# Performance work log

Hardware: AMD Instinct MI355X
Metric: run time of the kernel (lower is better)

## Reference

```python
import jax, jax.numpy as jnp
import numpy as np

B, N, D = 32, 4096, 128
H = D // 2      # GRU hidden = 64
Q = D // 4      # MLP hidden = 32
HORIZON = 28


def setup_inputs() -> dict:
    key = jax.random.key(0)
    ks = jax.random.split(key, 16)
    s = lambda k, shape, fan: jax.random.normal(k, shape, jnp.float32) * (1.0 / np.sqrt(fan))
    return {
        "features": jax.random.normal(ks[0], (B, N, D), jnp.float32),
        "last_value": jax.random.uniform(ks[1], (B, N), jnp.float32),
        # GRU (input_size=1, hidden=H), PyTorch gate order r,z,n
        "W_ih": s(ks[2], (3 * H, 1), 1),
        "W_hh": s(ks[3], (3 * H, H), H),
        "b_ih": s(ks[4], (3 * H,), H),
        "b_hh": s(ks[5], (3 * H,), H),
        # hidden_proj: Linear(D -> H)
        "Wp": s(ks[6], (H, D), D), "bp": s(ks[7], (H,), D),
        # output_proj: Linear(H->Q), ReLU, Linear(Q->1)
        "Wo1": s(ks[8], (Q, H), H), "bo1": s(ks[9], (Q,), H),
        "Wo2": s(ks[10], (1, Q), Q), "bo2": s(ks[11], (1,), Q),
        # refine_gate: Linear(D->Q), ReLU, Linear(Q->horizon), Sigmoid
        "Wg1": s(ks[12], (Q, D), D), "bg1": s(ks[13], (Q,), D),
        "Wg2": s(ks[14], (HORIZON, Q), Q), "bg2": s(ks[15], (HORIZON,), Q),
        "log_decay": jnp.asarray(-2.3, jnp.float32),
    }


def reference(features, last_value, W_ih, W_hh, b_ih, b_hh, Wp, bp,
              Wo1, bo1, Wo2, bo2, Wg1, bg1, Wg2, bg2, log_decay):
    b, n, d = features.shape
    h0 = features.reshape(b * n, d) @ Wp.T + bp          # [BN, H]
    x0 = last_value.reshape(b * n, 1)                    # [BN, 1]

    def step(carry, _):
        h, x = carry
        gi = x @ W_ih.T + b_ih                           # [BN, 3H]
        gh = h @ W_hh.T + b_hh                           # [BN, 3H]
        r = jax.nn.sigmoid(gi[:, :H] + gh[:, :H])
        z = jax.nn.sigmoid(gi[:, H:2 * H] + gh[:, H:2 * H])
        ncell = jnp.tanh(gi[:, 2 * H:] + r * gh[:, 2 * H:])
        h_new = (1.0 - z) * ncell + z * h
        pred = jax.nn.relu(h_new @ Wo1.T + bo1) @ Wo2.T + bo2  # [BN, 1] (dropout = eval)
        return (h_new, pred), pred[:, 0]

    (_, _), preds = jax.lax.scan(step, (h0, x0), None, length=HORIZON)
    gru_pred = preds.T.reshape(b, n, HORIZON)            # [B, N, horizon]

    gate = jax.nn.sigmoid(jax.nn.relu(features @ Wg1.T + bg1) @ Wg2.T + bg2)
    t = jnp.arange(1, HORIZON + 1, dtype=jnp.float32)
    decay_curve = jnp.exp(-jnp.exp(log_decay) * t)       # [horizon]
    decay_pred = last_value[..., None] * decay_curve
    return gate * gru_pred + (1.0 - gate) * decay_pred
```

## Files before the change

kernel.cpp:

```cpp
#include <hip/hip_runtime.h>

#define TPB 256
#define HOR 28
#define LOG2E 1.44269504088896340736f

typedef _Float16 f16;
typedef __attribute__((ext_vector_type(2))) _Float16 f16x2;
typedef __attribute__((ext_vector_type(4))) _Float16 f16x4;
typedef __attribute__((ext_vector_type(8))) _Float16 f16x8;
typedef __attribute__((ext_vector_type(4))) float f32x4;

union V8 { f16x8 v8; f16x4 v4[2]; f16x2 h2[4]; };

#define MFMA16(A,B,C) __builtin_amdgcn_mfma_f32_16x16x32_f16((A),(B),(C),0,0,0)

__device__ __forceinline__ f16x2 pk2(float a, float b) {
    return __builtin_bit_cast(f16x2, __builtin_amdgcn_cvt_pkrtz(a, b));
}

#define WS 68

__global__ __launch_bounds__(TPB, 4) void predictor_kernel(
    const float* __restrict__ features,
    const float* __restrict__ last_value,
    const float* __restrict__ W_ih,
    const float* __restrict__ W_hh,
    const float* __restrict__ b_ih,
    const float* __restrict__ b_hh,
    const float* __restrict__ Wp,
    const float* __restrict__ bp,
    const float* __restrict__ Wo1,
    const float* __restrict__ bo1,
    const float* __restrict__ Wo2,
    const float* __restrict__ bo2,
    const float* __restrict__ Wg1,
    const float* __restrict__ bg1,
    const float* __restrict__ Wg2,
    const float* __restrict__ bg2,
    const float* __restrict__ log_decay,
    float* __restrict__ out)
{
    __shared__ __align__(16) f16 s_mem[16000];

    const int tid = threadIdx.x;
    const int wv = tid >> 6, ln = tid & 63;
    const int a = ln & 15, g = ln >> 4;
    const int row0 = blockIdx.x * 64 + wv * 16;

    const f32x4 ZF = {0.f, 0.f, 0.f, 0.f};
    const f16x2 Z2 = {(f16)0.f, (f16)0.f};
    const f16x4 ZH4 = {(f16)0.f, (f16)0.f, (f16)0.f, (f16)0.f};

    f16* s_wp  = s_mem;
    f16* s_wg1 = s_mem + 8704;
    f16* s_wg2 = s_mem + 13056;

    for (int i = tid; i < 64 * 128; i += TPB) s_wp [(i >> 7) * 136 + (i & 127)] = (f16)Wp[i];
    for (int i = tid; i < 32 * 128; i += TPB) s_wg1[(i >> 7) * 136 + (i & 127)] = (f16)Wg1[i];
    for (int i = tid; i < 32 * 32; i += TPB) {
        int t = i >> 5, s = i & 31;
        int q = ((s >> 2) & 1) * 16 + ((s >> 3) & 3) * 4 + (s & 3);
        s_wg2[t * 40 + s] = (f16)((t < HOR) ? Wg2[t * 32 + q] : 0.0f);
    }

    f16x2 bH[4][2];
    #pragma unroll
    for (int c = 0; c < 4; ++c)
        #pragma unroll
        for (int p = 0; p < 2; ++p) {
            int u0 = c * 16 + g * 4 + 2 * p;
            bH[c][p] = pk2(b_hh[128 + u0] * 2.0f * LOG2E, b_hh[128 + u0 + 1] * 2.0f * LOG2E);
        }
    f16x2 bo1q[2][2], wo2q[2][2];
    #pragma unroll
    for (int mt = 0; mt < 2; ++mt)
        #pragma unroll
        for (int p = 0; p < 2; ++p) {
            int q0 = mt * 16 + g * 4 + 2 * p;
            bo1q[mt][p] = pk2(bo1[q0], bo1[q0 + 1]);
            wo2q[mt][p] = pk2(Wo2[q0], Wo2[q0 + 1]);
        }
    const float bo2v = bo2[0];
    const float edc  = LOG2E * __builtin_amdgcn_exp2f(LOG2E * log_decay[0]);
    const float lv   = last_value[row0 + a];
    const bool  g0   = (g == 0);

    V8 FF[4];
    #pragma unroll
    for (int kt = 0; kt < 4; ++kt) {
        const float* fp = features + (size_t)(row0 + a) * 128 + kt * 32 + g * 8;
        f32x4 v0 = *(const f32x4*)fp;
        f32x4 v1 = *(const f32x4*)(fp + 4);
        FF[kt].h2[0] = pk2(v0[0], v0[1]); FF[kt].h2[1] = pk2(v0[2], v0[3]);
        FF[kt].h2[2] = pk2(v1[0], v1[1]); FF[kt].h2[3] = pk2(v1[2], v1[3]);
    }

    __syncthreads();

    f32x4 h4[4];
    {
        f16x2 bpq[4][2];
        #pragma unroll
        for (int c = 0; c < 4; ++c)
            #pragma unroll
            for (int p = 0; p < 2; ++p) {
                int u0 = c * 16 + g * 4 + 2 * p;
                bpq[c][p] = pk2(bp[u0], bp[u0 + 1]);
            }
        #pragma unroll
        for (int nt = 0; nt < 4; ++nt) {
            f32x4 acc = ZF;
            #pragma unroll
            for (int kt = 0; kt < 4; ++kt) {
                f16x8 w = *(const f16x8*)&s_wp[(nt * 16 + a) * 136 + kt * 32 + g * 8];
                acc = MFMA16(w, FF[kt].v8, acc);
            }
            #pragma unroll
            for (int r = 0; r < 4; ++r) acc[r] += (float)bpq[nt][r >> 1][r & 1];
            h4[nt] = acc;
        }
    }

    float gA0, gA1, gA2, gA3, gB0, gB1, gB2, gB3;
    {
        f32x4 a1acc[2];
        #pragma unroll
        for (int mt = 0; mt < 2; ++mt) {
            f32x4 acc = ZF;
            #pragma unroll
            for (int kt = 0; kt < 4; ++kt) {
                f16x8 w = *(const f16x8*)&s_wg1[(mt * 16 + a) * 136 + kt * 32 + g * 8];
                acc = MFMA16(w, FF[kt].v8, acc);
            }
            #pragma unroll
            for (int r = 0; r < 4; ++r) {
                int q0 = mt * 16 + g * 4 + r;
                acc[r] = fmaxf(acc[r] + bg1[q0], 0.f);
            }
            a1acc[mt] = acc;
        }
        V8 A1;
        A1.h2[0] = pk2(a1acc[0][0], a1acc[0][1]);
        A1.h2[1] = pk2(a1acc[0][2], a1acc[0][3]);
        A1.h2[2] = pk2(a1acc[1][0], a1acc[1][1]);
        A1.h2[3] = pk2(a1acc[1][2], a1acc[1][3]);
        float gv[2][4];
        #pragma unroll
        for (int mt = 0; mt < 2; ++mt) {
            f32x4 acc = ZF;
            f16x8 w = *(const f16x8*)&s_wg2[(mt * 16 + a) * 40 + g * 8];
            acc = MFMA16(w, A1.v8, acc);
            #pragma unroll
            for (int r = 0; r < 4; ++r) {
                int t0 = mt * 16 + g * 4 + r;
                float lg = acc[r] + ((t0 < HOR) ? bg2[t0] : 0.f);
                gv[mt][r] = __builtin_amdgcn_rcpf(1.0f + __builtin_amdgcn_exp2f(-LOG2E * lg));
            }
        }
        gA0 = gv[0][0]; gA1 = gv[0][1]; gA2 = gv[0][2]; gA3 = gv[0][3];
        gB0 = gv[1][0]; gB1 = gv[1][1]; gB2 = gv[1][2]; gB3 = gv[1][3];
    }

    __syncthreads();
    f16* s_whh = s_mem;
    f16* s_wo1 = s_mem + 13056;
    f16* s_wx  = s_mem + 15232;
    for (int i = tid; i < 192 * WS; i += TPB) {
        int rr = i / WS, cc = i - rr * WS;
        float s = (rr < 128) ? -LOG2E : 2.0f * LOG2E;
        s_whh[i] = (f16)((cc < 64) ? W_hh[rr * 64 + cc] * s : 0.0f);
    }
    for (int i = tid; i < 32 * WS; i += TPB) {
        int rr = i / WS, cc = i - rr * WS;
        s_wo1[i] = (f16)((cc < 64) ? Wo1[rr * 64 + cc] : 0.0f);
    }
    for (int i = tid; i < 192; i += TPB) {
        float s = (i < 128) ? -LOG2E : 2.0f * LOG2E;
        s_wx[i * 4 + 0] = (f16)(W_ih[i] * s);
        s_wx[i * 4 + 1] = (f16)(((i < 128) ? (b_ih[i] + b_hh[i]) : b_ih[i]) * s);
        s_wx[i * 4 + 2] = (f16)0.f;
        s_wx[i * 4 + 3] = (f16)0.f;
    }
    __syncthreads();

    const int wr = a * WS + 4 * g;

    V8 F0, F1, F2;
    F0.h2[0] = pk2(h4[0][0], h4[0][1]); F0.h2[1] = pk2(h4[0][2], h4[0][3]);
    F0.h2[2] = pk2(h4[1][0], h4[1][1]); F0.h2[3] = pk2(h4[1][2], h4[1][3]);
    F1.h2[0] = pk2(h4[2][0], h4[2][1]); F1.h2[1] = pk2(h4[2][2], h4[2][3]);
    F1.h2[2] = pk2(h4[3][0], h4[3][1]); F1.h2[3] = pk2(h4[3][2], h4[3][3]);
    F2.h2[0] = Z2; F2.h2[1] = Z2; F2.h2[2] = Z2; F2.h2[3] = Z2;

    float x = lv;

#define GATE3(ACC, BR, c) do { \
        V8 w0_, w1_, w2_; \
        const int rw_ = BR + (c) * 16 + a; \
        const int rb_ = (BR + (c) * 16) * WS + wr; \
        w0_.v4[0] = *(const f16x4*)&s_whh[rb_]; \
        w0_.v4[1] = *(const f16x4*)&s_whh[rb_ + 16]; \
        w1_.v4[0] = *(const f16x4*)&s_whh[rb_ + 32]; \
        w1_.v4[1] = *(const f16x4*)&s_whh[rb_ + 48]; \
        w2_.v4[0] = *(const f16x4*)&s_wx[rw_ * 4]; \
        w2_.v4[1] = ZH4; \
        ACC = MFMA16(w0_.v8, F0.v8, ZF); \
        ACC = MFMA16(w1_.v8, F1.v8, ACC); \
        ACC = MFMA16(w2_.v8, F2.v8, ACC); } while (0)

#define GATEN(ACC, ACC2, c) do { \
        V8 w0_, w1_, w2_; \
        const int rw_ = 128 + (c) * 16 + a; \
        const int rb_ = (128 + (c) * 16) * WS + wr; \
        w0_.v4[0] = *(const f16x4*)&s_whh[rb_]; \
        w0_.v4[1] = *(const f16x4*)&s_whh[rb_ + 16]; \
        w1_.v4[0] = *(const f16x4*)&s_whh[rb_ + 32]; \
        w1_.v4[1] = *(const f16x4*)&s_whh[rb_ + 48]; \
        w2_.v4[0] = *(const f16x4*)&s_wx[rw_ * 4]; \
        w2_.v4[1] = ZH4; \
        ACC = MFMA16(w0_.v8, F0.v8, ZF); \
        ACC = MFMA16(w1_.v8, F1.v8, ACC); \
        ACC2 = MFMA16(w2_.v8, F2.v8, ZF); } while (0)

#define GRU_CELL(c, AR, AZ, AN, AN2) do { \
        _Pragma("unroll") \
        for (int p = 0; p < 2; ++p) { \
            _Pragma("unroll") \
            for (int q = 0; q < 2; ++q) { \
                int r = p * 2 + q; \
                float rg = __builtin_amdgcn_rcpf(1.0f + __builtin_amdgcn_exp2f(AR[r])); \
                float pb = 1.0f + __builtin_amdgcn_exp2f(AZ[r]); \
                float ghn = AN[r] + (float)bH[c][p][q]; \
                float E  = __builtin_amdgcn_exp2f(fmaf(rg, ghn, AN2[r])); \
                float pE = 1.0f + E; \
                float rD = __builtin_amdgcn_rcpf(pb * pE); \
                float zg = rD * pE; \
                float ivE = rD * pb; \
                float nc = fmaf(-2.0f, ivE, 1.0f); \
                float hv = h4[c][r]; \
                h4[c][r] = fmaf(zg, hv - nc, nc); \
            } \
        } } while (0)

    #pragma unroll 1
    for (int t = 0; t < HOR; ++t) {
        asm volatile("" ::: "memory");
        f16x2 x1 = pk2(x, 1.0f);
        F2.h2[0] = g0 ? x1 : Z2;

        f32x4 aR0, aZ0, aN0, aN20, aR1, aZ1, aN1, aN21;
        GATE3(aR0, 0, 0); GATE3(aZ0, 64, 0); GATEN(aN0, aN20, 0);
        GATE3(aR1, 0, 1); GATE3(aZ1, 64, 1); GATEN(aN1, aN21, 1);
        GRU_CELL(0, aR0, aZ0, aN0, aN20);
        GRU_CELL(1, aR1, aZ1, aN1, aN21);
        GATE3(aR0, 0, 2); GATE3(aZ0, 64, 2); GATEN(aN0, aN20, 2);
        GATE3(aR1, 0, 3); GATE3(aZ1, 64, 3); GATEN(aN1, aN21, 3);
        GRU_CELL(2, aR0, aZ0, aN0, aN20);
        GRU_CELL(3, aR1, aZ1, aN1, aN21);

        F0.h2[0] = pk2(h4[0][0], h4[0][1]); F0.h2[1] = pk2(h4[0][2], h4[0][3]);
        F0.h2[2] = pk2(h4[1][0], h4[1][1]); F0.h2[3] = pk2(h4[1][2], h4[1][3]);
        F1.h2[0] = pk2(h4[2][0], h4[2][1]); F1.h2[1] = pk2(h4[2][2], h4[2][3]);
        F1.h2[2] = pk2(h4[3][0], h4[3][1]); F1.h2[3] = pk2(h4[3][2], h4[3][3]);

        V8 wo;
        f32x4 o0 = ZF, o1 = ZF;
        wo.v4[0] = *(const f16x4*)&s_wo1[wr];
        wo.v4[1] = *(const f16x4*)&s_wo1[wr + 16];
        o0 = MFMA16(wo.v8, F0.v8, o0);
        wo.v4[0] = *(const f16x4*)&s_wo1[wr + 32];
        wo.v4[1] = *(const f16x4*)&s_wo1[wr + 48];
        o0 = MFMA16(wo.v8, F1.v8, o0);
        wo.v4[0] = *(const f16x4*)&s_wo1[16 * WS + wr];
        wo.v4[1] = *(const f16x4*)&s_wo1[16 * WS + wr + 16];
        o1 = MFMA16(wo.v8, F0.v8, o1);
        wo.v4[0] = *(const f16x4*)&s_wo1[16 * WS + wr + 32];
        wo.v4[1] = *(const f16x4*)&s_wo1[16 * WS + wr + 48];
        o1 = MFMA16(wo.v8, F1.v8, o1);

        float part = 0.f;
        #pragma unroll
        for (int p = 0; p < 2; ++p)
            #pragma unroll
            for (int q = 0; q < 2; ++q) {
                int r = 2 * p + q;
                part += fmaxf(o0[r] + (float)bo1q[0][p][q], 0.f) * (float)wo2q[0][p][q];
                part += fmaxf(o1[r] + (float)bo1q[1][p][q], 0.f) * (float)wo2q[1][p][q];
            }
        part += __shfl_xor(part, 16);
        part += __shfl_xor(part, 32);
        float pred = part + bo2v;

        if (g == ((t >> 2) & 3)) {
            float s01 = (t & 1) ? ((t & 16) ? gB1 : gA1) : ((t & 16) ? gB0 : gA0);
            float s23 = (t & 1) ? ((t & 16) ? gB3 : gA3) : ((t & 16) ? gB2 : gA2);
            float gvf = (t & 2) ? s23 : s01;
            float dc = __builtin_amdgcn_exp2f(-edc * (float)(t + 1));
            float lvdc = lv * dc;
            out[(size_t)(row0 + a) * HOR + t] = fmaf(gvf, pred - lvdc, lvdc);
        }
        x = pred;
    }
#undef GATE3
#undef GATEN
#undef GRU_CELL
}

extern "C" void kernel_launch(void* const* d_in, const int* in_sizes, int n_in,
                              void* d_out, int out_size, void* d_ws, size_t ws_size,
                              hipStream_t stream) {
    const float* features   = (const float*)d_in[0];
    const float* last_value = (const float*)d_in[1];
    const float* W_ih       = (const float*)d_in[2];
    const float* W_hh       = (const float*)d_in[3];
    const float* b_ih       = (const float*)d_in[4];
    const float* b_hh       = (const float*)d_in[5];
    const float* Wp         = (const float*)d_in[6];
    const float* bp         = (const float*)d_in[7];
    const float* Wo1        = (const float*)d_in[8];
    const float* bo1        = (const float*)d_in[9];
    const float* Wo2        = (const float*)d_in[10];
    const float* bo2        = (const float*)d_in[11];
    const float* Wg1        = (const float*)d_in[12];
    const float* bg1        = (const float*)d_in[13];
    const float* Wg2        = (const float*)d_in[14];
    const float* bg2        = (const float*)d_in[15];
    const float* log_decay  = (const float*)d_in[16];
    float* out = (float*)d_out;

    dim3 grid(131072 / 64), block(TPB);
    predictor_kernel<<<grid, block, 0, stream>>>(
        features, last_value, W_ih, W_hh, b_ih, b_hh, Wp, bp,
        Wo1, bo1, Wo2, bo2, Wg1, bg1, Wg2, bg2, log_decay, out);
}
```

Measured before the change: 257.1 us.

## Process two 16-row tiles per wave to reuse GRU weight loads

```diff
diff --git a/kernel.cpp b/kernel.cpp
--- a/kernel.cpp
+++ b/kernel.cpp
@@ -17,10 +17,13 @@
 __device__ __forceinline__ f16x2 pk2(float a, float b) {
     return __builtin_bit_cast(f16x2, __builtin_amdgcn_cvt_pkrtz(a, b));
 }
+__device__ __forceinline__ float sigm_pos(float lg) {
+    return __builtin_amdgcn_rcpf(1.0f + __builtin_amdgcn_exp2f(-LOG2E * lg));
+}
 
 #define WS 68
 
-__global__ __launch_bounds__(TPB, 4) void predictor_kernel(
+__global__ __launch_bounds__(TPB, 3) void predictor_kernel(
     const float* __restrict__ features,
     const float* __restrict__ last_value,
     const float* __restrict__ W_ih,
@@ -45,7 +48,7 @@
     const int tid = threadIdx.x;
     const int wv = tid >> 6, ln = tid & 63;
     const int a = ln & 15, g = ln >> 4;
-    const int row0 = blockIdx.x * 64 + wv * 16;
+    const int row0 = blockIdx.x * 128 + wv * 32;
 
     const f32x4 ZF = {0.f, 0.f, 0.f, 0.f};
     const f16x2 Z2 = {(f16)0.f, (f16)0.f};
@@ -82,84 +85,86 @@
         }
     const float bo2v = bo2[0];
     const float edc  = LOG2E * __builtin_amdgcn_exp2f(LOG2E * log_decay[0]);
-    const float lv   = last_value[row0 + a];
+    const float lvA  = last_value[row0 + a];
+    const float lvB  = last_value[row0 + 16 + a];
     const bool  g0   = (g == 0);
 
-    V8 FF[4];
-    #pragma unroll
-    for (int kt = 0; kt < 4; ++kt) {
-        const float* fp = features + (size_t)(row0 + a) * 128 + kt * 32 + g * 8;
-        f32x4 v0 = *(const f32x4*)fp;
-        f32x4 v1 = *(const f32x4*)(fp + 4);
-        FF[kt].h2[0] = pk2(v0[0], v0[1]); FF[kt].h2[1] = pk2(v0[2], v0[3]);
-        FF[kt].h2[2] = pk2(v1[0], v1[1]); FF[kt].h2[3] = pk2(v1[2], v1[3]);
-    }
-
     __syncthreads();
 
-    f32x4 h4[4];
-    {
-        f16x2 bpq[4][2];
-        #pragma unroll
-        for (int c = 0; c < 4; ++c)
-            #pragma unroll
-            for (int p = 0; p < 2; ++p) {
-                int u0 = c * 16 + g * 4 + 2 * p;
-                bpq[c][p] = pk2(bp[u0], bp[u0 + 1]);
-            }
-        #pragma unroll
-        for (int nt = 0; nt < 4; ++nt) {
-            f32x4 acc = ZF;
-            #pragma unroll
-            for (int kt = 0; kt < 4; ++kt) {
-                f16x8 w = *(const f16x8*)&s_wp[(nt * 16 + a) * 136 + kt * 32 + g * 8];
-                acc = MFMA16(w, FF[kt].v8, acc);
-            }
-            #pragma unroll
-            for (int r = 0; r < 4; ++r) acc[r] += (float)bpq[nt][r >> 1][r & 1];
-            h4[nt] = acc;
-        }
-    }
-
-    float gA0, gA1, gA2, gA3, gB0, gB1, gB2, gB3;
-    {
-        f32x4 a1acc[2];
-        #pragma unroll
-        for (int mt = 0; mt < 2; ++mt) {
-            f32x4 acc = ZF;
-            #pragma unroll
-            for (int kt = 0; kt < 4; ++kt) {
-                f16x8 w = *(const f16x8*)&s_wg1[(mt * 16 + a) * 136 + kt * 32 + g * 8];
-                acc = MFMA16(w, FF[kt].v8, acc);
-            }
-            #pragma unroll
-            for (int r = 0; r < 4; ++r) {
-                int q0 = mt * 16 + g * 4 + r;
-                acc[r] = fmaxf(acc[r] + bg1[q0], 0.f);
-            }
-            a1acc[mt] = acc;
-        }
-        V8 A1;
-        A1.h2[0] = pk2(a1acc[0][0], a1acc[0][1]);
-        A1.h2[1] = pk2(a1acc[0][2], a1acc[0][3]);
-        A1.h2[2] = pk2(a1acc[1][0], a1acc[1][1]);
-        A1.h2[3] = pk2(a1acc[1][2], a1acc[1][3]);
-        float gv[2][4];
-        #pragma unroll
-        for (int mt = 0; mt < 2; ++mt) {
-            f32x4 acc = ZF;
-            f16x8 w = *(const f16x8*)&s_wg2[(mt * 16 + a) * 40 + g * 8];
-            acc = MFMA16(w, A1.v8, acc);
-            #pragma unroll
-            for (int r = 0; r < 4; ++r) {
-                int t0 = mt * 16 + g * 4 + r;
-                float lg = acc[r] + ((t0 < HOR) ? bg2[t0] : 0.f);
-                gv[mt][r] = __builtin_amdgcn_rcpf(1.0f + __builtin_amdgcn_exp2f(-LOG2E * lg));
-            }
-        }
-        gA0 = gv[0][0]; gA1 = gv[0][1]; gA2 = gv[0][2]; gA3 = gv[0][3];
-        gB0 = gv[1][0]; gB1 = gv[1][1]; gB2 = gv[1][2]; gB3 = gv[1][3];
-    }
+    f32x4 h4A[4], h4B[4];
+    float ga0, ga1, ga2, ga3, ga4, ga5, ga6, ga7;
+    float gb0, gb1, gb2, gb3, gb4, gb5, gb6, gb7;
+
+#define PHASE1(H4, G0_, G1_, G2_, G3_, G4_, G5_, G6_, G7_, ROFF) do { \
+    V8 FF0, FF1, FF2, FF3; \
+    { \
+        const float* fb_ = features + (size_t)(row0 + (ROFF) + a) * 128 + g * 8; \
+        f32x4 v0, v1; \
+        v0 = *(const f32x4*)(fb_);       v1 = *(const f32x4*)(fb_ + 4); \
+        FF0.h2[0]=pk2(v0[0],v0[1]); FF0.h2[1]=pk2(v0[2],v0[3]); FF0.h2[2]=pk2(v1[0],v1[1]); FF0.h2[3]=pk2(v1[2],v1[3]); \
+        v0 = *(const f32x4*)(fb_ + 32);  v1 = *(const f32x4*)(fb_ + 36); \
+        FF1.h2[0]=pk2(v0[0],v0[1]); FF1.h2[1]=pk2(v0[2],v0[3]); FF1.h2[2]=pk2(v1[0],v1[1]); FF1.h2[3]=pk2(v1[2],v1[3]); \
+        v0 = *(const f32x4*)(fb_ + 64);  v1 = *(const f32x4*)(fb_ + 68); \
+        FF2.h2[0]=pk2(v0[0],v0[1]); FF2.h2[1]=pk2(v0[2],v0[3]); FF2.h2[2]=pk2(v1[0],v1[1]); FF2.h2[3]=pk2(v1[2],v1[3]); \
+        v0 = *(const f32x4*)(fb_ + 96);  v1 = *(const f32x4*)(fb_ + 100); \
+        FF3.h2[0]=pk2(v0[0],v0[1]); FF3.h2[1]=pk2(v0[2],v0[3]); FF3.h2[2]=pk2(v1[0],v1[1]); FF3.h2[3]=pk2(v1[2],v1[3]); \
+    } \
+    _Pragma("unroll") \
+    for (int nt = 0; nt < 4; ++nt) { \
+        f32x4 acc = ZF; \
+        const f16* wp_ = &s_wp[(nt * 16 + a) * 136 + g * 8]; \
+        acc = MFMA16(*(const f16x8*)(wp_),       FF0.v8, acc); \
+        acc = MFMA16(*(const f16x8*)(wp_ + 32),  FF1.v8, acc); \
+        acc = MFMA16(*(const f16x8*)(wp_ + 64),  FF2.v8, acc); \
+        acc = MFMA16(*(const f16x8*)(wp_ + 96),  FF3.v8, acc); \
+        _Pragma("unroll") \
+        for (int r = 0; r < 4; ++r) acc[r] += bp[nt * 16 + g * 4 + r]; \
+        H4[nt] = acc; \
+    } \
+    f32x4 a1_0, a1_1; \
+    { \
+        f32x4 acc = ZF; \
+        const f16* wg_ = &s_wg1[a * 136 + g * 8]; \
+        acc = MFMA16(*(const f16x8*)(wg_),       FF0.v8, acc); \
+        acc = MFMA16(*(const f16x8*)(wg_ + 32),  FF1.v8, acc); \
+        acc = MFMA16(*(const f16x8*)(wg_ + 64),  FF2.v8, acc); \
+        acc = MFMA16(*(const f16x8*)(wg_ + 96),  FF3.v8, acc); \
+        _Pragma("unroll") \
+        for (int r = 0; r < 4; ++r) acc[r] = fmaxf(acc[r] + bg1[g * 4 + r], 0.f); \
+        a1_0 = acc; \
+    } \
+    { \
+        f32x4 acc = ZF; \
+        const f16* wg_ = &s_wg1[(16 + a) * 136 + g * 8]; \
+        acc = MFMA16(*(const f16x8*)(wg_),       FF0.v8, acc); \
+        acc = MFMA16(*(const f16x8*)(wg_ + 32),  FF1.v8, acc); \
+        acc = MFMA16(*(const f16x8*)(wg_ + 64),  FF2.v8, acc); \
+        acc = MFMA16(*(const f16x8*)(wg_ + 96),  FF3.v8, acc); \
+        _Pragma("unroll") \
+        for (int r = 0; r < 4; ++r) acc[r] = fmaxf(acc[r] + bg1[16 + g * 4 + r], 0.f); \
+        a1_1 = acc; \
+    } \
+    V8 A1_; \
+    A1_.h2[0] = pk2(a1_0[0], a1_0[1]); A1_.h2[1] = pk2(a1_0[2], a1_0[3]); \
+    A1_.h2[2] = pk2(a1_1[0], a1_1[1]); A1_.h2[3] = pk2(a1_1[2], a1_1[3]); \
+    { \
+        f32x4 ac0 = ZF, ac1 = ZF; \
+        ac0 = MFMA16(*(const f16x8*)&s_wg2[a * 40 + g * 8],        A1_.v8, ac0); \
+        ac1 = MFMA16(*(const f16x8*)&s_wg2[(16 + a) * 40 + g * 8], A1_.v8, ac1); \
+        G0_ = sigm_pos(ac0[0] + bg2[g * 4 + 0]); \
+        G1_ = sigm_pos(ac0[1] + bg2[g * 4 + 1]); \
+        G2_ = sigm_pos(ac0[2] + bg2[g * 4 + 2]); \
+        G3_ = sigm_pos(ac0[3] + bg2[g * 4 + 3]); \
+        int t4_ = 16 + g * 4; \
+        G4_ = sigm_pos(ac1[0] + ((t4_ + 0 < HOR) ? bg2[t4_ + 0] : 0.f)); \
+        G5_ = sigm_pos(ac1[1] + ((t4_ + 1 < HOR) ? bg2[t4_ + 1] : 0.f)); \
+        G6_ = sigm_pos(ac1[2] + ((t4_ + 2 < HOR) ? bg2[t4_ + 2] : 0.f)); \
+        G7_ = sigm_pos(ac1[3] + ((t4_ + 3 < HOR) ? bg2[t4_ + 3] : 0.f)); \
+    } } while (0)
+
+    PHASE1(h4A, ga0, ga1, ga2, ga3, ga4, ga5, ga6, ga7, 0);
+    PHASE1(h4B, gb0, gb1, gb2, gb3, gb4, gb5, gb6, gb7, 16);
+#undef PHASE1
 
     __syncthreads();
     f16* s_whh = s_mem;
@@ -185,44 +190,52 @@
 
     const int wr = a * WS + 4 * g;
 
-    V8 F0, F1, F2;
-    F0.h2[0] = pk2(h4[0][0], h4[0][1]); F0.h2[1] = pk2(h4[0][2], h4[0][3]);
-    F0.h2[2] = pk2(h4[1][0], h4[1][1]); F0.h2[3] = pk2(h4[1][2], h4[1][3]);
-    F1.h2[0] = pk2(h4[2][0], h4[2][1]); F1.h2[1] = pk2(h4[2][2], h4[2][3]);
-    F1.h2[2] = pk2(h4[3][0], h4[3][1]); F1.h2[3] = pk2(h4[3][2], h4[3][3]);
-    F2.h2[0] = Z2; F2.h2[1] = Z2; F2.h2[2] = Z2; F2.h2[3] = Z2;
-
-    float x = lv;
-
-#define GATE3(ACC, BR, c) do { \
+    V8 F0A, F1A, F0B, F1B, F2A, F2B;
+#define PACKF(F0_, F1_, H4) do { \
+    F0_.h2[0] = pk2(H4[0][0], H4[0][1]); F0_.h2[1] = pk2(H4[0][2], H4[0][3]); \
+    F0_.h2[2] = pk2(H4[1][0], H4[1][1]); F0_.h2[3] = pk2(H4[1][2], H4[1][3]); \
+    F1_.h2[0] = pk2(H4[2][0], H4[2][1]); F1_.h2[1] = pk2(H4[2][2], H4[2][3]); \
+    F1_.h2[2] = pk2(H4[3][0], H4[3][1]); F1_.h2[3] = pk2(H4[3][2], H4[3][3]); } while (0)
+    PACKF(F0A, F1A, h4A);
+    PACKF(F0B, F1B, h4B);
+    F2A.h2[0] = Z2; F2A.h2[1] = Z2; F2A.h2[2] = Z2; F2A.h2[3] = Z2;
+    F2B.h2[0] = Z2; F2B.h2[1] = Z2; F2B.h2[2] = Z2; F2B.h2[3] = Z2;
+
+    float xA = lvA, xB = lvB;
+
+#define GATE3_2(ACCA, ACCB, BR, c) do { \
         V8 w0_, w1_, w2_; \
-        const int rw_ = BR + (c) * 16 + a; \
         const int rb_ = (BR + (c) * 16) * WS + wr; \
         w0_.v4[0] = *(const f16x4*)&s_whh[rb_]; \
         w0_.v4[1] = *(const f16x4*)&s_whh[rb_ + 16]; \
         w1_.v4[0] = *(const f16x4*)&s_whh[rb_ + 32]; \
         w1_.v4[1] = *(const f16x4*)&s_whh[rb_ + 48]; \
-        w2_.v4[0] = *(const f16x4*)&s_wx[rw_ * 4]; \
+        w2_.v4[0] = *(const f16x4*)&s_wx[(BR + (c) * 16 + a) * 4]; \
         w2_.v4[1] = ZH4; \
-        ACC = MFMA16(w0_.v8, F0.v8, ZF); \
-        ACC = MFMA16(w1_.v8, F1.v8, ACC); \
-        ACC = MFMA16(w2_.v8, F2.v8, ACC); } while (0)
-
-#define GATEN(ACC, ACC2, c) do { \
+        ACCA = MFMA16(w0_.v8, F0A.v8, ZF); \
+        ACCB = MFMA16(w0_.v8, F0B.v8, ZF); \
+        ACCA = MFMA16(w1_.v8, F1A.v8, ACCA); \
+        ACCB = MFMA16(w1_.v8, F1B.v8, ACCB); \
+        ACCA = MFMA16(w2_.v8, F2A.v8, ACCA); \
+        ACCB = MFMA16(w2_.v8, F2B.v8, ACCB); } while (0)
+
+#define GATEN_2(ACCA, ACC2A, ACCB, ACC2B, c) do { \
         V8 w0_, w1_, w2_; \
-        const int rw_ = 128 + (c) * 16 + a; \
         const int rb_ = (128 + (c) * 16) * WS + wr; \
         w0_.v4[0] = *(const f16x4*)&s_whh[rb_]; \
         w0_.v4[1] = *(const f16x4*)&s_whh[rb_ + 16]; \
         w1_.v4[0] = *(const f16x4*)&s_whh[rb_ + 32]; \
         w1_.v4[1] = *(const f16x4*)&s_whh[rb_ + 48]; \
-        w2_.v4[0] = *(const f16x4*)&s_wx[rw_ * 4]; \
+        w2_.v4[0] = *(const f16x4*)&s_wx[(128 + (c) * 16 + a) * 4]; \
         w2_.v4[1] = ZH4; \
-        ACC = MFMA16(w0_.v8, F0.v8, ZF); \
-        ACC = MFMA16(w1_.v8, F1.v8, ACC); \
-        ACC2 = MFMA16(w2_.v8, F2.v8, ZF); } while (0)
-
-#define GRU_CELL(c, AR, AZ, AN, AN2) do { \
+        ACCA = MFMA16(w0_.v8, F0A.v8, ZF); \
+        ACCB = MFMA16(w0_.v8, F0B.v8, ZF); \
+        ACCA = MFMA16(w1_.v8, F1A.v8, ACCA); \
+        ACCB = MFMA16(w1_.v8, F1B.v8, ACCB); \
+        ACC2A = MFMA16(w2_.v8, F2A.v8, ZF); \
+        ACC2B = MFMA16(w2_.v8, F2B.v8, ZF); } while (0)
+
+#define GRU_CELL(H4, c, AR, AZ, AN, AN2) do { \
         _Pragma("unroll") \
         for (int p = 0; p < 2; ++p) { \
             _Pragma("unroll") \
@@ -237,73 +250,84 @@
                 float zg = rD * pE; \
                 float ivE = rD * pb; \
                 float nc = fmaf(-2.0f, ivE, 1.0f); \
-                float hv = h4[c][r]; \
-                h4[c][r] = fmaf(zg, hv - nc, nc); \
+                float hv = H4[c][r]; \
+                H4[c][r] = fmaf(zg, hv - nc, nc); \
             } \
         } } while (0)
 
     #pragma unroll 1
     for (int t = 0; t < HOR; ++t) {
         asm volatile("" ::: "memory");
-        f16x2 x1 = pk2(x, 1.0f);
-        F2.h2[0] = g0 ? x1 : Z2;
-
-        f32x4 aR0, aZ0, aN0, aN20, aR1, aZ1, aN1, aN21;
-        GATE3(aR0, 0, 0); GATE3(aZ0, 64, 0); GATEN(aN0, aN20, 0);
-        GATE3(aR1, 0, 1); GATE3(aZ1, 64, 1); GATEN(aN1, aN21, 1);
-        GRU_CELL(0, aR0, aZ0, aN0, aN20);
-        GRU_CELL(1, aR1, aZ1, aN1, aN21);
-        GATE3(aR0, 0, 2); GATE3(aZ0, 64, 2); GATEN(aN0, aN20, 2);
-        GATE3(aR1, 0, 3); GATE3(aZ1, 64, 3); GATEN(aN1, aN21, 3);
-        GRU_CELL(2, aR0, aZ0, aN0, aN20);
-        GRU_CELL(3, aR1, aZ1, aN1, aN21);
-
-        F0.h2[0] = pk2(h4[0][0], h4[0][1]); F0.h2[1] = pk2(h4[0][2], h4[0][3]);
-        F0.h2[2] = pk2(h4[1][0], h4[1][1]); F0.h2[3] = pk2(h4[1][2], h4[1][3]);
-        F1.h2[0] = pk2(h4[2][0], h4[2][1]); F1.h2[1] = pk2(h4[2][2], h4[2][3]);
-        F1.h2[2] = pk2(h4[3][0], h4[3][1]); F1.h2[3] = pk2(h4[3][2], h4[3][3]);
+        F2A.h2[0] = g0 ? pk2(xA, 1.0f) : Z2;
+        F2B.h2[0] = g0 ? pk2(xB, 1.0f) : Z2;
+
+        #pragma unroll
+        for (int c = 0; c < 4; ++c) {
+            f32x4 aRA, aZA, aNA, aN2A, aRB, aZB, aNB, aN2B;
+            GATE3_2(aRA, aRB, 0, c);
+            GATE3_2(aZA, aZB, 64, c);
+            GATEN_2(aNA, aN2A, aNB, aN2B, c);
+            GRU_CELL(h4A, c, aRA, aZA, aNA, aN2A);
+            GRU_CELL(h4B, c, aRB, aZB, aNB, aN2B);
+        }
+
+        PACKF(F0A, F1A, h4A);
+        PACKF(F0B, F1B, h4B);
 
         V8 wo;
-        f32x4 o0 = ZF, o1 = ZF;
+        f32x4 o0A = ZF, o1A = ZF, o0B = ZF, o1B = ZF;
         wo.v4[0] = *(const f16x4*)&s_wo1[wr];
         wo.v4[1] = *(const f16x4*)&s_wo1[wr + 16];
-        o0 = MFMA16(wo.v8, F0.v8, o0);
+        o0A = MFMA16(wo.v8, F0A.v8, o0A); o0B = MFMA16(wo.v8, F0B.v8, o0B);
         wo.v4[0] = *(const f16x4*)&s_wo1[wr + 32];
         wo.v4[1] = *(const f16x4*)&s_wo1[wr + 48];
-        o0 = MFMA16(wo.v8, F1.v8, o0);
+        o0A = MFMA16(wo.v8, F1A.v8, o0A); o0B = MFMA16(wo.v8, F1B.v8, o0B);
         wo.v4[0] = *(const f16x4*)&s_wo1[16 * WS + wr];
         wo.v4[1] = *(const f16x4*)&s_wo1[16 * WS + wr + 16];
-        o1 = MFMA16(wo.v8, F0.v8, o1);
+        o1A = MFMA16(wo.v8, F0A.v8, o1A); o1B = MFMA16(wo.v8, F0B.v8, o1B);
         wo.v4[0] = *(const f16x4*)&s_wo1[16 * WS + wr + 32];
         wo.v4[1] = *(const f16x4*)&s_wo1[16 * WS + wr + 48];
-        o1 = MFMA16(wo.v8, F1.v8, o1);
-
-        float part = 0.f;
+        o1A = MFMA16(wo.v8, F1A.v8, o1A); o1B = MFMA16(wo.v8, F1B.v8, o1B);
+
+        float partA = 0.f, partB = 0.f;
         #pragma unroll
         for (int p = 0; p < 2; ++p)
             #pragma unroll
             for (int q = 0; q < 2; ++q) {
                 int r = 2 * p + q;
-                part += fmaxf(o0[r] + (float)bo1q[0][p][q], 0.f) * (float)wo2q[0][p][q];
-                part += fmaxf(o1[r] + (float)bo1q[1][p][q], 0.f) * (float)wo2q[1][p][q];
+                partA += fmaxf(o0A[r] + (float)bo1q[0][p][q], 0.f) * (float)wo2q[0][p][q];
+                partA += fmaxf(o1A[r] + (float)bo1q[1][p][q], 0.f) * (float)wo2q[1][p][q];
+                partB += fmaxf(o0B[r] + (float)bo1q[0][p][q], 0.f) * (float)wo2q[0][p][q];
+                partB += fmaxf(o1B[r] + (float)bo1q[1][p][q], 0.f) * (float)wo2q[1][p][q];
             }
-        part += __shfl_xor(part, 16);
-        part += __shfl_xor(part, 32);
-        float pred = part + bo2v;
+        partA += __shfl_xor(partA, 16);
+        partA += __shfl_xor(partA, 32);
+        partB += __shfl_xor(partB, 16);
+        partB += __shfl_xor(partB, 32);
+        float predA = partA + bo2v;
+        float predB = partB + bo2v;
 
         if (g == ((t >> 2) & 3)) {
-            float s01 = (t & 1) ? ((t & 16) ? gB1 : gA1) : ((t & 16) ? gB0 : gA0);
-            float s23 = (t & 1) ? ((t & 16) ? gB3 : gA3) : ((t & 16) ? gB2 : gA2);
-            float gvf = (t & 2) ? s23 : s01;
             float dc = __builtin_amdgcn_exp2f(-edc * (float)(t + 1));
-            float lvdc = lv * dc;
-            out[(size_t)(row0 + a) * HOR + t] = fmaf(gvf, pred - lvdc, lvdc);
+            float s01, s23, gvf;
+            s01 = (t & 1) ? ((t & 16) ? ga5 : ga1) : ((t & 16) ? ga4 : ga0);
+            s23 = (t & 1) ? ((t & 16) ? ga7 : ga3) : ((t & 16) ? ga6 : ga2);
+            gvf = (t & 2) ? s23 : s01;
+            float lvdcA = lvA * dc;
+            out[(size_t)(row0 + a) * HOR + t] = fmaf(gvf, predA - lvdcA, lvdcA);
+            s01 = (t & 1) ? ((t & 16) ? gb5 : gb1) : ((t & 16) ? gb4 : gb0);
+            s23 = (t & 1) ? ((t & 16) ? gb7 : gb3) : ((t & 16) ? gb6 : gb2);
+            gvf = (t & 2) ? s23 : s01;
+            float lvdcB = lvB * dc;
+            out[(size_t)(row0 + 16 + a) * HOR + t] = fmaf(gvf, predB - lvdcB, lvdcB);
         }
-        x = pred;
-    }
-#undef GATE3
-#undef GATEN
+        xA = predA;
+        xB = predB;
+    }
+#undef GATE3_2
+#undef GATEN_2
 #undef GRU_CELL
+#undef PACKF
 }
 
 extern "C" void kernel_launch(void* const* d_in, const int* in_sizes, int n_in,
@@ -328,7 +352,7 @@
     const float* log_decay  = (const float*)d_in[16];
     float* out = (float*)d_out;
 
-    dim3 grid(131072 / 64), block(TPB);
+    dim3 grid(131072 / 128), block(TPB);
     predictor_kernel<<<grid, block, 0, stream>>>(
         features, last_value, W_ih, W_hh, b_ih, b_hh, Wp, bp,
         Wo1, bo1, Wo2, bo2, Wg1, bg1, Wg2, bg2, log_decay, out);
```

Measured after the change: 280.9 us. 1.09x slower.
